# Kernel tuning notes

Measured on AMD Instinct MI355X. Metric: run time of the kernel, lower is better.

The kernel has to match this reference:

```python
import jax, jax.numpy as jnp
import numpy as np

B, H, N, D, C, G = 4, 4, 4096, 256, 256, 64  # batch, heads, tokens, emb, channels, grid
EPS = 1e-5


def _layernorm(x, g, b):
    mu = jnp.mean(x, axis=-1, keepdims=True)
    var = jnp.var(x, axis=-1, keepdims=True)
    return (x - mu) * jax.lax.rsqrt(var + EPS) * g + b


def setup_inputs() -> dict:
    key = jax.random.key(0)
    ks = jax.random.split(key, 24)
    s = lambda fan_in: 1.0 / np.sqrt(fan_in)
    inp = {
        "img_emb": jax.random.normal(ks[0], (B, C, G, G), jnp.float32),
        "point_emb": jax.random.normal(ks[1], (B, N, D), jnp.float32),
        # stacked per-head projections (torch Linear: y = x @ W.T + b; store W already transposed)
        "Wq": jax.random.uniform(ks[2], (H, D, D), jnp.float32, -s(D), s(D)),
        "bq": jax.random.uniform(ks[3], (H, D), jnp.float32, -s(D), s(D)),
        "Wk": jax.random.uniform(ks[4], (H, C, D), jnp.float32, -s(C), s(C)),
        "bk": jax.random.uniform(ks[5], (H, D), jnp.float32, -s(C), s(C)),
        "Wv": jax.random.uniform(ks[6], (H, C, D), jnp.float32, -s(C), s(C)),
        "bv": jax.random.uniform(ks[7], (H, D), jnp.float32, -s(C), s(C)),
        "Wo": jax.random.uniform(ks[8], (H * D, D), jnp.float32, -s(H * D), s(H * D)),
        "bo": jax.random.uniform(ks[9], (D,), jnp.float32, -s(H * D), s(H * D)),
        "pos": jax.random.normal(ks[10], (N, D), jnp.float32),
        # FF: 256->128->64->1
        "W1": jax.random.uniform(ks[11], (256, 128), jnp.float32, -s(256), s(256)),
        "b1": jax.random.uniform(ks[12], (128,), jnp.float32, -s(256), s(256)),
        "g1": jnp.ones((128,), jnp.float32),
        "be1": jnp.zeros((128,), jnp.float32),
        "W2": jax.random.uniform(ks[13], (128, 64), jnp.float32, -s(128), s(128)),
        "b2": jax.random.uniform(ks[14], (64,), jnp.float32, -s(128), s(128)),
        "g2": jnp.ones((64,), jnp.float32),
        "be2": jnp.zeros((64,), jnp.float32),
        "W3": jax.random.uniform(ks[15], (64, 1), jnp.float32, -s(64), s(64)),
        "b3": jax.random.uniform(ks[16], (1,), jnp.float32, -s(64), s(64)),
    }
    return inp


def reference(img_emb, point_emb, Wq, bq, Wk, bk, Wv, bv, Wo, bo, pos,
              W1, b1, g1, be1, W2, b2, g2, be2, W3, b3):
    b = img_emb.shape[0]
    # [B, C, G, G] -> [B, N, C]
    img = jnp.transpose(img_emb, (0, 2, 3, 1)).reshape(b, -1, img_emb.shape[1])
    img_pos = img + pos[None, :, :]
    # batched per-head QKV (collapses the per-head Python loop)
    q = jnp.einsum('bnd,hde->bhne', point_emb, Wq) + bq[None, :, None, :]
    k = jnp.einsum('bnc,hce->bhne', img, Wk) + bk[None, :, None, :]
    v = jnp.einsum('bnc,hce->bhne', img_pos, Wv) + bv[None, :, None, :]
    scores = jnp.einsum('bhqe,bhke->bhqk', q, k) / jnp.sqrt(jnp.float32(D))
    attn = jax.nn.softmax(scores, axis=-1)
    att = jnp.einsum('bhqk,bhke->bhqe', attn, v)          # [B, H, N, E]
    att = jnp.transpose(att, (0, 2, 1, 3)).reshape(b, N, H * D)  # concat heads
    emb = att @ Wo + bo + point_emb                        # residual, [B, N, D]
    # small FFN head
    h = _layernorm(jax.nn.relu(emb @ W1 + b1), g1, be1)
    h = _layernorm(jax.nn.relu(h @ W2 + b2), g2, be2)
    act = jax.nn.sigmoid(h @ W3 + b3)                      # [B, N, 1]
    return act, emb
```

## Files before the change

kernel.cpp:

```cpp
#include <hip/hip_runtime.h>

typedef __attribute__((ext_vector_type(8))) short bfrag;
typedef __attribute__((ext_vector_type(8))) unsigned short us8;
typedef __attribute__((ext_vector_type(16))) float f16v;

__device__ __forceinline__ unsigned short f2bf(float f) {
  union { float f; unsigned u; } v; v.f = f;
  unsigned u = v.u;
  return (unsigned short)((u + 0x7fffu + ((u >> 16) & 1u)) >> 16);
}
__device__ __forceinline__ unsigned pkbf(float a, float b) {
  return (unsigned)f2bf(a) | ((unsigned)f2bf(b) << 16);
}
__device__ __forceinline__ float wred(float v) {
#pragma unroll
  for (int m = 32; m >= 1; m >>= 1) v += __shfl_xor(v, m, 64);
  return v;
}
__device__ __forceinline__ void dma16(const void* g, void* l) {
  __builtin_amdgcn_global_load_lds(
      (const __attribute__((address_space(1))) void*)g,
      (__attribute__((address_space(3))) void*)l, 16, 0, 0);
}

__device__ __forceinline__ void transp64(
    const float* __restrict__ inz, unsigned short* __restrict__ oz,
    int R, int Cc, int i0, int j0, int tid)
{
  int l = tid & 63, ty = tid >> 6;
  int i = i0 + l;
#pragma unroll
  for (int itr = 0; itr < 2; ++itr) {
    int j = j0 + ty * 16 + itr * 8;
    const float* p = inz + (long)i * Cc + j;
    float4 v0 = *(const float4*)(p);
    float4 v1 = *(const float4*)(p + 4);
    float vv[8] = {v0.x, v0.y, v0.z, v0.w, v1.x, v1.y, v1.z, v1.w};
#pragma unroll
    for (int s = 0; s < 8; ++s) oz[(long)(j + s) * R + i] = f2bf(vv[s]);
  }
}

__global__ __launch_bounds__(256) void prep_kernel(
    const float* __restrict__ point_emb, short* __restrict__ peT,
    const float* __restrict__ img_emb, const float* __restrict__ pos,
    short* __restrict__ imgT, short* __restrict__ imgPosT,
    const float* __restrict__ Wq, const float* __restrict__ Wk,
    const float* __restrict__ Wv, short* __restrict__ WqT,
    const float* __restrict__ Wo, short* __restrict__ WoT)
{
  __shared__ float tile[64][65];
  int b = blockIdx.x;
  int tid = threadIdx.x;

  if (b < 2048) {
    long i = ((long)b * 256 + tid) * 8;
    float4 v0 = *(const float4*)(point_emb + i);
    float4 v1 = *(const float4*)(point_emb + i + 4);
    uint4 st;
    st.x = pkbf(v0.x, v0.y);
    st.y = pkbf(v0.z, v0.w);
    st.z = pkbf(v1.x, v1.y);
    st.w = pkbf(v1.z, v1.w);
    *(uint4*)((unsigned short*)peT + i) = st;
  } else if (b < 3072) {
    int bb = b - 2048;
    int x = bb & 63, y = (bb >> 6) & 3, z = bb >> 8;
    long zofs = (long)z * (256L * 4096L);
    const float* inz = img_emb + zofs;
    int i0 = y * 64, j0 = x * 64;
    int r0 = (tid >> 6) * 16, c = tid & 63;
#pragma unroll
    for (int rr = 0; rr < 16; ++rr) {
      tile[c][r0 + rr] = inz[(long)(i0 + r0 + rr) * 4096 + j0 + c];
    }
    __syncthreads();
    unsigned short* o1 = (unsigned short*)imgT + zofs;
    unsigned short* o2 = (unsigned short*)imgPosT + zofs;
#pragma unroll
    for (int rr = 0; rr < 16; ++rr) {
      int tt = r0 + rr;
      float v = tile[tt][c];
      long o = (long)(j0 + tt) * 256 + i0 + c;
      o1[o] = f2bf(v);
      o2[o] = f2bf(v + pos[o]);
    }
  } else if (b < 3264) {
    int bb = b - 3072;
    int x = bb & 3, y = (bb >> 2) & 3, z = bb >> 4;
    const float* inz = (z < 4 ? Wq : (z < 8 ? Wk : Wv)) + (long)(z & 3) * 65536;
    unsigned short* oz = (unsigned short*)WqT + (long)z * 65536;
    transp64(inz, oz, 256, 256, x * 64, y * 64, tid);
  } else {
    int bb = b - 3264;
    int x = bb & 15, y = bb >> 4;
    transp64(Wo, (unsigned short*)WoT, 1024, 256, x * 64, y * 64, tid);
  }
}

__global__ __launch_bounds__(256) void gemm_qk(
    const short* __restrict__ Aq, const short* __restrict__ Btq,
    const float* __restrict__ biasq, short* __restrict__ Cq,
    const short* __restrict__ Ak, const short* __restrict__ Btk,
    const float* __restrict__ biask, short* __restrict__ Ck,
    float qscale)
{
  int idg = blockIdx.x;
  int sel = idg >> 11;
  int id = idg & 2047;
  const short* A  = sel ? Ak : Aq;
  const short* Bt = sel ? Btk : Btq;
  const float* bias = sel ? biask : biasq;
  short* Co = sel ? Ck : Cq;
  float scale = sel ? 1.0f : qscale;

  int y = id & 3, h = (id >> 2) & 3;
  int g = id >> 4;
  int xt = g & 31, bsel = g >> 5;
  int z = bsel * 4 + h;

  const short* Az = A + (long)bsel * 1048576;
  const short* Btz = Bt + (long)h * 65536;
  const float* biasz = bias + (long)h * 256;
  short* Cz = Co + (long)z * 1048576;

  int tid = threadIdx.x;
  int w = tid >> 6, lane = tid & 63;
  int half = lane >> 5, ln = lane & 31;
  int wm = w & 1, wn = w >> 1;
  int row0 = xt * 128 + wm * 64;
  int col0 = y * 64 + wn * 32;

  f16v acc0, acc1;
#pragma unroll
  for (int i = 0; i < 16; ++i) { acc0[i] = 0.f; acc1[i] = 0.f; }

  const short* ap0 = Az + (long)(row0 + ln) * 256 + half * 8;
  const short* ap1 = Az + (long)(row0 + 32 + ln) * 256 + half * 8;
  const short* bp  = Btz + (long)(col0 + ln) * 256 + half * 8;

#pragma unroll
  for (int kt = 0; kt < 16; ++kt) {
    bfrag a0 = *(const bfrag*)(ap0 + kt * 16);
    bfrag a1 = *(const bfrag*)(ap1 + kt * 16);
    bfrag bbv = *(const bfrag*)(bp + kt * 16);
    acc0 = __builtin_amdgcn_mfma_f32_32x32x16_bf16(a0, bbv, acc0, 0, 0, 0);
    acc1 = __builtin_amdgcn_mfma_f32_32x32x16_bf16(a1, bbv, acc1, 0, 0, 0);
  }

  int col = col0 + ln;
  float bv = biasz[col];
#pragma unroll
  for (int t = 0; t < 2; ++t) {
    int rbase = row0 + t * 32;
#pragma unroll
    for (int r = 0; r < 16; ++r) {
      float av = t ? acc1[r] : acc0[r];
      int rr = rbase + (r & 3) + 8 * (r >> 2) + 4 * half;
      ((unsigned short*)Cz)[(long)rr * 256 + col] = f2bf((av + bv) * scale);
    }
  }
}

__global__ __launch_bounds__(256) void gemm_v(
    const short* __restrict__ A, const short* __restrict__ Bt,
    const float* __restrict__ bias, short* __restrict__ Co)
{
  int id = blockIdx.x;
  int y = id & 3, h = (id >> 2) & 3;
  int g = id >> 4;
  int xt = g & 31, bsel = g >> 5;
  int z = bsel * 4 + h;

  const short* Az = A + (long)bsel * 1048576;
  const short* Btz = Bt + (long)h * 65536;
  const float* biasz = bias + (long)h * 256;
  short* Cz = Co + (long)z * 1048576;

  int tid = threadIdx.x;
  int w = tid >> 6, lane = tid & 63;
  int half = lane >> 5, ln = lane & 31;
  int wm = w & 1, wn = w >> 1;
  int row0 = xt * 128 + wm * 64;
  int col0 = y * 64 + wn * 32;

  f16v acc0, acc1;
#pragma unroll
  for (int i = 0; i < 16; ++i) { acc0[i] = 0.f; acc1[i] = 0.f; }

  const short* ap0 = Az + (long)(row0 + ln) * 256 + half * 8;
  const short* ap1 = Az + (long)(row0 + 32 + ln) * 256 + half * 8;
  const short* bp  = Btz + (long)(col0 + ln) * 256 + half * 8;

#pragma unroll
  for (int kt = 0; kt < 16; ++kt) {
    bfrag a0 = *(const bfrag*)(ap0 + kt * 16);
    bfrag a1 = *(const bfrag*)(ap1 + kt * 16);
    bfrag bbv = *(const bfrag*)(bp + kt * 16);
    acc0 = __builtin_amdgcn_mfma_f32_32x32x16_bf16(a0, bbv, acc0, 0, 0, 0);
    acc1 = __builtin_amdgcn_mfma_f32_32x32x16_bf16(a1, bbv, acc1, 0, 0, 0);
  }

  int col = col0 + ln;
  float bv = biasz[col];
#pragma unroll
  for (int t = 0; t < 2; ++t) {
    int rbase = row0 + t * 32;
#pragma unroll
    for (int g2 = 0; g2 < 4; ++g2) {
      float v0 = (t ? acc1[4*g2+0] : acc0[4*g2+0]) + bv;
      float v1 = (t ? acc1[4*g2+1] : acc0[4*g2+1]) + bv;
      float v2 = (t ? acc1[4*g2+2] : acc0[4*g2+2]) + bv;
      float v3 = (t ? acc1[4*g2+3] : acc0[4*g2+3]) + bv;
      uint2 st;
      st.x = pkbf(v0, v1);
      st.y = pkbf(v2, v3);
      *(uint2*)&((unsigned short*)Cz)[(long)col * 4096 + rbase + 8 * g2 + 4 * half] = st;
    }
  }
}

__global__ __launch_bounds__(256) void gemm_out(
    const short* __restrict__ A, const short* __restrict__ Bt,
    const float* __restrict__ bias, float* __restrict__ Co,
    const float* __restrict__ resid)
{
  int id = blockIdx.x;
  int xt = id >> 2, y = id & 3;

  int tid = threadIdx.x;
  int w = tid >> 6, lane = tid & 63;
  int half = lane >> 5, ln = lane & 31;
  int wm = w & 1, wn = w >> 1;
  int row0 = xt * 128 + wm * 64;
  int col0 = y * 64 + wn * 32;

  f16v acc0, acc1;
#pragma unroll
  for (int i = 0; i < 16; ++i) { acc0[i] = 0.f; acc1[i] = 0.f; }

  int r0 = row0 + ln, r1 = row0 + 32 + ln;
  long a0base = (long)(r0 >> 12) * 4194304 + (long)(r0 & 4095) * 256 + half * 8;
  long a1base = (long)(r1 >> 12) * 4194304 + (long)(r1 & 4095) * 256 + half * 8;
  const short* bp = Bt + (long)(col0 + ln) * 1024 + half * 8;

  for (int kh = 0; kh < 4; ++kh) {
    const short* a0p = A + a0base + (long)kh * 1048576;
    const short* a1p = A + a1base + (long)kh * 1048576;
    const short* bkp = bp + kh * 256;
#pragma unroll
    for (int kt = 0; kt < 16; ++kt) {
      bfrag a0 = *(const bfrag*)(a0p + kt * 16);
      bfrag a1 = *(const bfrag*)(a1p + kt * 16);
      bfrag bbv = *(const bfrag*)(bkp + kt * 16);
      acc0 = __builtin_amdgcn_mfma_f32_32x32x16_bf16(a0, bbv, acc0, 0, 0, 0);
      acc1 = __builtin_amdgcn_mfma_f32_32x32x16_bf16(a1, bbv, acc1, 0, 0, 0);
    }
  }

  int col = col0 + ln;
  float bv = bias[col];
#pragma unroll
  for (int t = 0; t < 2; ++t) {
    int rbase = row0 + t * 32;
#pragma unroll
    for (int r = 0; r < 16; ++r) {
      float av = t ? acc1[r] : acc0[r];
      int rr = rbase + (r & 3) + 8 * (r >> 2) + 4 * half;
      Co[(long)rr * 256 + col] = av + bv + resid[(long)rr * 256 + col];
    }
  }
}

__global__ __launch_bounds__(512, 2) void attn_kernel(
    const short* __restrict__ Qg, const short* __restrict__ Kg,
    const short* __restrict__ Vtg, short* __restrict__ attc)
{
  __shared__ char smem[131072];
  int bx = blockIdx.x;
  int bh = bx & 15, qg = bx >> 4;
  int tid = threadIdx.x;
  int w = tid >> 6, lane = tid & 63;
  int half = lane >> 5, ln = lane & 31;
  int q0 = qg * 256 + w * 32;

  bfrag qf[8];
  int qoff = 65536 + w * 8192 + lane * 16;
  {
    const short* qrow = Qg + ((long)bh * 4096 + q0 + ln) * 256 + half * 8;
#pragma unroll
    for (int kt = 0; kt < 8; ++kt) qf[kt] = *(const bfrag*)(qrow + kt * 16);
#pragma unroll
    for (int kt = 8; kt < 16; ++kt) {
      us8 v = *(const us8*)(qrow + kt * 16);
      *(us8*)(smem + qoff + (kt - 8) * 1024) = v;
    }
  }

  int koff[4], voff[2];
#pragma unroll
  for (int m = 0; m < 4; ++m) koff[m] = ((ln ^ (2 * m + half)) * 16) + half * 512;
#pragma unroll
  for (int kp = 0; kp < 2; ++kp) {
    int ck = 2 * kp + half;
    voff[kp] = 16384 + ck * 4096 + ((ln ^ (ck << 1)) * 16);
  }

  int w2 = w * 2;
  int kgl0, kgl1, vgl0, vgl1;
  {
    int c0 = w2 * 2 + half;
    kgl0 = (ln ^ (c0 & 7)) * 512 + c0 * 16;
    int c1 = (w2 + 1) * 2 + half;
    kgl1 = (ln ^ (c1 & 7)) * 512 + c1 * 16;
    int ck0 = w2 >> 2;
    int e0 = ((w2 & 3) * 64 + lane) ^ (ck0 << 1);
    vgl0 = e0 * 8192 + ck0 * 16;
    int ck1 = (w2 + 1) >> 2;
    int e1 = (((w2 + 1) & 3) * 64 + lane) ^ (ck1 << 1);
    vgl1 = e1 * 8192 + ck1 * 16;
  }
  const char* kgp = (const char*)Kg + (long)bh * 2097152;
  const char* vgp = (const char*)Vtg + (long)bh * 2097152;

  f16v O[8];
#pragma unroll
  for (int t = 0; t < 8; ++t)
#pragma unroll
    for (int r = 0; r < 16; ++r) O[t][r] = 0.f;

  float l_run = 0.f;
  union { bfrag f; unsigned u[4]; } bb[2];
  f16v SA, SB;

#define PACK_BB(kp, SV)                                                        \
  {                                                                            \
    unsigned q0_, q1_, q2_, q3_;                                               \
    asm("v_cvt_pk_bf16_f32 %0, %1, %2"                                         \
        : "=v"(q0_) : "v"(SV[8*(kp)+0]), "v"(SV[8*(kp)+1]));                   \
    asm("v_cvt_pk_bf16_f32 %0, %1, %2"                                         \
        : "=v"(q1_) : "v"(SV[8*(kp)+2]), "v"(SV[8*(kp)+3]));                   \
    asm("v_cvt_pk_bf16_f32 %0, %1, %2"                                         \
        : "=v"(q2_) : "v"(SV[8*(kp)+4]), "v"(SV[8*(kp)+5]));                   \
    asm("v_cvt_pk_bf16_f32 %0, %1, %2"                                         \
        : "=v"(q3_) : "v"(SV[8*(kp)+6]), "v"(SV[8*(kp)+7]));                   \
    asm("v_permlane32_swap_b32 %0, %1" : "+v"(q0_), "+v"(q2_));                \
    asm("v_permlane32_swap_b32 %0, %1" : "+v"(q1_), "+v"(q3_));                \
    bb[kp].u[0] = q0_;                                                         \
    bb[kp].u[1] = q1_;                                                         \
    bb[kp].u[2] = q2_;                                                         \
    bb[kp].u[3] = q3_;                                                         \
  }

#define SOFTMAX_BB(SV)                                                         \
  {                                                                            \
    float ss = 0.f;                                                            \
    _Pragma("unroll")                                                          \
    for (int r = 0; r < 16; ++r) { float e = exp2f(SV[r] - 8.f); SV[r] = e; ss += e; } \
    l_run += ss;                                                               \
    PACK_BB(0, SV)                                                             \
    PACK_BB(1, SV)                                                             \
  }

#define SCHAIN(BUF, SNEW)                                                      \
  {                                                                            \
    _Pragma("unroll")                                                          \
    for (int r = 0; r < 16; ++r) SNEW[r] = 0.f;                                \
    _Pragma("unroll")                                                          \
    for (int kt = 0; kt < 8; ++kt) {                                           \
      bfrag a = *(const bfrag*)(smem + koff[kt & 3] + ((BUF)*32768 + kt*1024));\
      SNEW = __builtin_amdgcn_mfma_f32_32x32x16_bf16(a, qf[kt], SNEW, 0, 0, 0);\
    }                                                                          \
    _Pragma("unroll")                                                          \
    for (int kt = 8; kt < 16; ++kt) {                                          \
      bfrag a = *(const bfrag*)(smem + koff[kt & 3] + ((BUF)*32768 + kt*1024));\
      bfrag qv = *(const bfrag*)(smem + qoff + (kt - 8) * 1024);               \
      SNEW = __builtin_amdgcn_mfma_f32_32x32x16_bf16(a, qv, SNEW, 0, 0, 0);    \
    }                                                                          \
  }

  dma16(kgp + kgl0, smem + w2 * 1024);
  dma16(kgp + kgl1, smem + (w2 + 1) * 1024);
  kgp += 16384;

  __syncthreads();
  dma16(kgp + kgl0, smem + 32768 + w2 * 1024);
  dma16(kgp + kgl1, smem + 32768 + (w2 + 1) * 1024);
  kgp += 16384;
  dma16(vgp + vgl0, smem + 32768 + 16384 + w2 * 1024);
  dma16(vgp + vgl1, smem + 32768 + 16384 + (w2 + 1) * 1024);
  vgp += 64;
  SCHAIN(0, SB)

#define ATTN_ITER(BUF, KLOAD, SNEW, SPREV)                                     \
  {                                                                            \
    __syncthreads();                                                           \
    if (KLOAD) {                                                               \
      dma16(kgp + kgl0, smem + ((BUF) ^ 1) * 32768 + w2 * 1024);               \
      dma16(kgp + kgl1, smem + ((BUF) ^ 1) * 32768 + (w2 + 1) * 1024);         \
      kgp += 16384;                                                            \
    }                                                                          \
    dma16(vgp + vgl0, smem + ((BUF) ^ 1) * 32768 + 16384 + w2 * 1024);         \
    dma16(vgp + vgl1, smem + ((BUF) ^ 1) * 32768 + 16384 + (w2 + 1) * 1024);   \
    vgp += 64;                                                                 \
    SCHAIN(BUF, SNEW)                                                          \
    SOFTMAX_BB(SPREV)                                                          \
    _Pragma("unroll")                                                          \
    for (int kt = 0; kt < 16; ++kt) {                                          \
      bfrag va = *(const bfrag*)(smem + voff[kt >> 3] +                        \
                                 ((BUF)*32768 + (kt & 7) * 512));              \
      O[kt & 7] = __builtin_amdgcn_mfma_f32_32x32x16_bf16(va, bb[kt >> 3].f,   \
                                                          O[kt & 7], 0, 0, 0); \
    }                                                                          \
  }

  for (int tp = 0; tp < 63; ++tp) {
    ATTN_ITER(1, 1, SA, SB)
    ATTN_ITER(0, 1, SB, SA)
  }
  ATTN_ITER(1, 0, SA, SB)

  __syncthreads();
  SOFTMAX_BB(SA)
#pragma unroll
  for (int kp = 0; kp < 2; ++kp) {
#pragma unroll
    for (int mt = 0; mt < 8; ++mt) {
      bfrag va = *(const bfrag*)(smem + voff[kp] + mt * 512);
      O[mt] = __builtin_amdgcn_mfma_f32_32x32x16_bf16(va, bb[kp].f, O[mt], 0, 0, 0);
    }
  }
#undef ATTN_ITER
#undef SCHAIN
#undef SOFTMAX_BB
#undef PACK_BB

  l_run += __shfl_xor(l_run, 32);
  float rl = 1.0f / l_run;
  short* orow = attc + ((long)bh * 4096 + q0 + ln) * 256;
#pragma unroll
  for (int mt = 0; mt < 8; ++mt) {
#pragma unroll
    for (int g = 0; g < 4; ++g) {
      uint2 st;
      st.x = pkbf(O[mt][4 * g + 0] * rl, O[mt][4 * g + 1] * rl);
      st.y = pkbf(O[mt][4 * g + 2] * rl, O[mt][4 * g + 3] * rl);
      *(uint2*)(orow + mt * 32 + 8 * g + 4 * half) = st;
    }
  }
}

__global__ __launch_bounds__(256) void ffn_kernel(
    const float* __restrict__ emb,
    const float* __restrict__ W1, const float* __restrict__ b1,
    const float* __restrict__ g1, const float* __restrict__ be1,
    const float* __restrict__ W2, const float* __restrict__ b2,
    const float* __restrict__ g2, const float* __restrict__ be2,
    const float* __restrict__ W3, const float* __restrict__ b3,
    float* __restrict__ act)
{
  __shared__ float xs[4][256][4];
  __shared__ float hs[4][128][4];
  int w = threadIdx.x >> 6, l = threadIdx.x & 63;
  int row0 = blockIdx.x * 16 + w * 4;
  const float* x = emb + (long)row0 * 256;

  {
    float xv[4][4];
#pragma unroll
    for (int rr = 0; rr < 4; ++rr) {
      float4 t = *(const float4*)(x + rr * 256 + 4 * l);
      xv[0][rr] = t.x; xv[1][rr] = t.y; xv[2][rr] = t.z; xv[3][rr] = t.w;
    }
#pragma unroll
    for (int i = 0; i < 4; ++i) {
      float4 st = make_float4(xv[i][0], xv[i][1], xv[i][2], xv[i][3]);
      *(float4*)&xs[w][4 * l + i][0] = st;
    }
  }

  float a0[4], a1[4];
  {
    float bb0 = b1[2 * l], bb1 = b1[2 * l + 1];
#pragma unroll
    for (int rr = 0; rr < 4; ++rr) { a0[rr] = bb0; a1[rr] = bb1; }
  }
  for (int k = 0; k < 256; ++k) {
    float w0 = W1[k * 128 + 2 * l], w1 = W1[k * 128 + 2 * l + 1];
    float4 xv = *(const float4*)&xs[w][k][0];
    a0[0] += xv.x * w0; a1[0] += xv.x * w1;
    a0[1] += xv.y * w0; a1[1] += xv.y * w1;
    a0[2] += xv.z * w0; a1[2] += xv.z * w1;
    a0[3] += xv.w * w0; a1[3] += xv.w * w1;
  }
  {
    float gg0 = g1[2 * l], gg1 = g1[2 * l + 1];
    float ee0 = be1[2 * l], ee1 = be1[2 * l + 1];
    float n0v[4], n1v[4];
#pragma unroll
    for (int rr = 0; rr < 4; ++rr) {
      float u0 = fmaxf(a0[rr], 0.f), u1 = fmaxf(a1[rr], 0.f);
      float s1 = wred(u0 + u1);
      float s2 = wred(u0 * u0 + u1 * u1);
      float mu = s1 * (1.f / 128.f);
      float var = fmaxf(s2 * (1.f / 128.f) - mu * mu, 0.f);
      float rs = rsqrtf(var + 1e-5f);
      n0v[rr] = (u0 - mu) * rs * gg0 + ee0;
      n1v[rr] = (u1 - mu) * rs * gg1 + ee1;
    }
    *(float4*)&hs[w][2 * l][0]     = make_float4(n0v[0], n0v[1], n0v[2], n0v[3]);
    *(float4*)&hs[w][2 * l + 1][0] = make_float4(n1v[0], n1v[1], n1v[2], n1v[3]);
  }

  float c0[4];
  {
    float bb2 = b2[l];
#pragma unroll
    for (int rr = 0; rr < 4; ++rr) c0[rr] = bb2;
  }
  for (int k = 0; k < 128; ++k) {
    float w2 = W2[k * 64 + l];
    float4 hv = *(const float4*)&hs[w][k][0];
    c0[0] += hv.x * w2;
    c0[1] += hv.y * w2;
    c0[2] += hv.z * w2;
    c0[3] += hv.w * w2;
  }
  {
    float gg2 = g2[l], ee2 = be2[l], w3 = W3[l], bb3 = b3[0];
#pragma unroll
    for (int rr = 0; rr < 4; ++rr) {
      float u = fmaxf(c0[rr], 0.f);
      float t1 = wred(u);
      float t2 = wred(u * u);
      float mu2 = t1 * (1.f / 64.f);
      float var2 = fmaxf(t2 * (1.f / 64.f) - mu2 * mu2, 0.f);
      float rs2 = rsqrtf(var2 + 1e-5f);
      float n2 = (u - mu2) * rs2 * gg2 + ee2;
      float tt = wred(n2 * w3);
      if (l == 0) {
        float r = tt + bb3;
        act[row0 + rr] = 1.f / (1.f + __expf(-r));
      }
    }
  }
}

extern "C" void kernel_launch(void* const* d_in, const int* in_sizes, int n_in,
                              void* d_out, int out_size, void* d_ws, size_t ws_size,
                              hipStream_t stream)
{
  const float* img_emb   = (const float*)d_in[0];
  const float* point_emb = (const float*)d_in[1];
  const float* Wq = (const float*)d_in[2];
  const float* bq = (const float*)d_in[3];
  const float* Wk = (const float*)d_in[4];
  const float* bk = (const float*)d_in[5];
  const float* Wv = (const float*)d_in[6];
  const float* bv = (const float*)d_in[7];
  const float* Wo = (const float*)d_in[8];
  const float* bo = (const float*)d_in[9];
  const float* pos = (const float*)d_in[10];
  const float* W1 = (const float*)d_in[11];
  const float* b1 = (const float*)d_in[12];
  const float* g1 = (const float*)d_in[13];
  const float* be1 = (const float*)d_in[14];
  const float* W2 = (const float*)d_in[15];
  const float* b2 = (const float*)d_in[16];
  const float* g2 = (const float*)d_in[17];
  const float* be2 = (const float*)d_in[18];
  const float* W3 = (const float*)d_in[19];
  const float* b3 = (const float*)d_in[20];

  char* ws = (char*)d_ws;
  short* Qb      = (short*)(ws + 0);
  short* Kb      = (short*)(ws + 33554432);
  short* VtB     = (short*)(ws + 67108864);
  short* peT     = (short*)(ws + 67108864);
  short* imgT    = (short*)(ws + 75497472);
  short* imgPosT = (short*)(ws + 100663296);
  short* WoT     = (short*)(ws + 109051904);
  short* WqT     = (short*)(ws + 109576192);
  short* WkT     = (short*)(ws + 110100480);
  short* WvT     = (short*)(ws + 110624768);
  (void)WkT; (void)WvT;

  float* act_out = (float*)d_out;
  float* emb_out = (float*)d_out + 16384;

  const float qscale = 0.0901684400555602f;

  prep_kernel<<<3328, 256, 0, stream>>>(point_emb, peT, img_emb, pos,
                                        imgT, imgPosT, Wq, Wk, Wv, WqT, Wo, WoT);

  gemm_qk<<<4096, 256, 0, stream>>>(peT, WqT, bq, Qb,
                                    imgT, WqT + 262144, bk, Kb, qscale);
  gemm_v<<<2048, 256, 0, stream>>>(imgPosT, WqT + 524288, bv, VtB);

  attn_kernel<<<256, 512, 0, stream>>>(Qb, Kb, VtB, Qb);

  gemm_out<<<512, 256, 0, stream>>>(Qb, WoT, bo, emb_out, point_emb);

  ffn_kernel<<<1024, 256, 0, stream>>>(emb_out, W1, b1, g1, be1, W2, b2, g2, be2,
                                       W3, b3, act_out);
}
```

Baseline: 611.9 us.

## Read K fragments directly from global memory instead of staging through LDS

The attention kernel no longer DMAs K tiles into shared memory. Each lane now loads its K MFMA fragments straight from global memory, advancing a pointer per 32-key tile. This shrinks LDS from 128KB to 96KB, which could help occupancy, and removes K's DMA and LDS traffic. The cost is uncoalesced, latency-exposed global loads on the critical path of the QK MFMA chain, with no prefetch, and K is re-read from L2 by every wave.

```diff
diff --git a/kernel.cpp b/kernel.cpp
--- a/kernel.cpp
+++ b/kernel.cpp
@@ -276,7 +276,7 @@
     const short* __restrict__ Qg, const short* __restrict__ Kg,
     const short* __restrict__ Vtg, short* __restrict__ attc)
 {
-  __shared__ char smem[131072];
+  __shared__ char smem[98304];
   int bx = blockIdx.x;
   int bh = bx & 15, qg = bx >> 4;
   int tid = threadIdx.x;
@@ -285,7 +285,7 @@
   int q0 = qg * 256 + w * 32;
 
   bfrag qf[8];
-  int qoff = 65536 + w * 8192 + lane * 16;
+  int qoff = 32768 + w * 8192 + lane * 16;
   {
     const short* qrow = Qg + ((long)bh * 4096 + q0 + ln) * 256 + half * 8;
 #pragma unroll
@@ -297,22 +297,18 @@
     }
   }
 
-  int koff[4], voff[2];
-#pragma unroll
-  for (int m = 0; m < 4; ++m) koff[m] = ((ln ^ (2 * m + half)) * 16) + half * 512;
+  int voff[2];
 #pragma unroll
   for (int kp = 0; kp < 2; ++kp) {
     int ck = 2 * kp + half;
-    voff[kp] = 16384 + ck * 4096 + ((ln ^ (ck << 1)) * 16);
-  }
+    voff[kp] = ck * 4096 + ((ln ^ (ck << 1)) * 16);
+  }
+
+  const short* kdir = Kg + ((long)bh * 4096 + ln) * 256 + half * 8;
 
   int w2 = w * 2;
-  int kgl0, kgl1, vgl0, vgl1;
-  {
-    int c0 = w2 * 2 + half;
-    kgl0 = (ln ^ (c0 & 7)) * 512 + c0 * 16;
-    int c1 = (w2 + 1) * 2 + half;
-    kgl1 = (ln ^ (c1 & 7)) * 512 + c1 * 16;
+  int vgl0, vgl1;
+  {
     int ck0 = w2 >> 2;
     int e0 = ((w2 & 3) * 64 + lane) ^ (ck0 << 1);
     vgl0 = e0 * 8192 + ck0 * 16;
@@ -320,7 +316,6 @@
     int e1 = (((w2 + 1) & 3) * 64 + lane) ^ (ck1 << 1);
     vgl1 = e1 * 8192 + ck1 * 16;
   }
-  const char* kgp = (const char*)Kg + (long)bh * 2097152;
   const char* vgp = (const char*)Vtg + (long)bh * 2097152;
 
   f16v O[8];
@@ -362,63 +357,51 @@
     PACK_BB(1, SV)                                                             \
   }
 
-#define SCHAIN(BUF, SNEW)                                                      \
+#define SCHAIN(SNEW)                                                           \
   {                                                                            \
     _Pragma("unroll")                                                          \
     for (int r = 0; r < 16; ++r) SNEW[r] = 0.f;                                \
     _Pragma("unroll")                                                          \
     for (int kt = 0; kt < 8; ++kt) {                                           \
-      bfrag a = *(const bfrag*)(smem + koff[kt & 3] + ((BUF)*32768 + kt*1024));\
+      bfrag a = *(const bfrag*)(kdir + kt * 16);                               \
       SNEW = __builtin_amdgcn_mfma_f32_32x32x16_bf16(a, qf[kt], SNEW, 0, 0, 0);\
     }                                                                          \
     _Pragma("unroll")                                                          \
     for (int kt = 8; kt < 16; ++kt) {                                          \
-      bfrag a = *(const bfrag*)(smem + koff[kt & 3] + ((BUF)*32768 + kt*1024));\
+      bfrag a = *(const bfrag*)(kdir + kt * 16);                               \
       bfrag qv = *(const bfrag*)(smem + qoff + (kt - 8) * 1024);               \
       SNEW = __builtin_amdgcn_mfma_f32_32x32x16_bf16(a, qv, SNEW, 0, 0, 0);    \
     }                                                                          \
-  }
-
-  dma16(kgp + kgl0, smem + w2 * 1024);
-  dma16(kgp + kgl1, smem + (w2 + 1) * 1024);
-  kgp += 16384;
-
-  __syncthreads();
-  dma16(kgp + kgl0, smem + 32768 + w2 * 1024);
-  dma16(kgp + kgl1, smem + 32768 + (w2 + 1) * 1024);
-  kgp += 16384;
-  dma16(vgp + vgl0, smem + 32768 + 16384 + w2 * 1024);
-  dma16(vgp + vgl1, smem + 32768 + 16384 + (w2 + 1) * 1024);
+    kdir += 8192;                       \
+  }
+
+  dma16(vgp + vgl0, smem + 16384 + w2 * 1024);
+  dma16(vgp + vgl1, smem + 16384 + (w2 + 1) * 1024);
   vgp += 64;
-  SCHAIN(0, SB)
-
-#define ATTN_ITER(BUF, KLOAD, SNEW, SPREV)                                     \
+  SCHAIN(SB)
+
+#define ATTN_ITER(BUF, SNEW, SPREV)                                            \
   {                                                                            \
     __syncthreads();                                                           \
-    if (KLOAD) {                                                               \
-      dma16(kgp + kgl0, smem + ((BUF) ^ 1) * 32768 + w2 * 1024);               \
-      dma16(kgp + kgl1, smem + ((BUF) ^ 1) * 32768 + (w2 + 1) * 1024);         \
-      kgp += 16384;                                                            \
-    }                                                                          \
-    dma16(vgp + vgl0, smem + ((BUF) ^ 1) * 32768 + 16384 + w2 * 1024);         \
-    dma16(vgp + vgl1, smem + ((BUF) ^ 1) * 32768 + 16384 + (w2 + 1) * 1024);   \
+    dma16(vgp + vgl0, smem + ((BUF) ^ 1) * 16384 + w2 * 1024);                 \
+    dma16(vgp + vgl1, smem + ((BUF) ^ 1) * 16384 + (w2 + 1) * 1024);           \
     vgp += 64;                                                                 \
-    SCHAIN(BUF, SNEW)                                                          \
+    SCHAIN(SNEW)                                                               \
     SOFTMAX_BB(SPREV)                                                          \
     _Pragma("unroll")                                                          \
     for (int kt = 0; kt < 16; ++kt) {                                          \
       bfrag va = *(const bfrag*)(smem + voff[kt >> 3] +                        \
-                                 ((BUF)*32768 + (kt & 7) * 512));              \
+                                 ((BUF)*16384 + (kt & 7) * 512));              \
       O[kt & 7] = __builtin_amdgcn_mfma_f32_32x32x16_bf16(va, bb[kt >> 3].f,   \
                                                           O[kt & 7], 0, 0, 0); \
     }                                                                          \
   }
 
   for (int tp = 0; tp < 63; ++tp) {
-    ATTN_ITER(1, 1, SA, SB)
-    ATTN_ITER(0, 1, SB, SA)
-  }
-  ATTN_ITER(1, 0, SA, SB)
+    ATTN_ITER(1, SA, SB)
+    ATTN_ITER(0, SB, SA)
+  }
+  ATTN_ITER(1, SA, SB)
 
   __syncthreads();
   SOFTMAX_BB(SA)
```

Result: slower. 1.185 ms (+93.6%).
